# Optimization experiments

Measured on AMD Instinct MI355X. Metric: run time of the kernel, lower is better.

Reference implementation:

```python
import jax, jax.numpy as jnp
import numpy as np

EMB = 768
HEADS = 12
HEAD_DIM = EMB // HEADS
SCALE = HEAD_DIM ** -0.5


def setup_inputs() -> dict:
    key = jax.random.key(0)
    kq, kk, kv, kw = jax.random.split(key, 4)
    B, H, N, D = 2, HEADS, 2048, HEAD_DIM
    queries = jax.random.normal(kq, (B, H, N, D), dtype=jnp.float32)
    keys = jax.random.normal(kk, (B, H, N, D), dtype=jnp.float32)
    values = jax.random.normal(kv, (B, H, N, D), dtype=jnp.float32)
    proj_w = jax.random.normal(kw, (EMB, EMB), dtype=jnp.float32) * (EMB ** -0.5)
    proj_b = jnp.zeros((EMB,), dtype=jnp.float32)
    return {"queries": queries, "keys": keys, "values": values,
            "proj_w": proj_w, "proj_b": proj_b}


def reference(queries, keys, values, proj_w, proj_b):
    # energy: [b, h, n, n] -- full quadratic score matrix, as in the original
    energy = jnp.einsum('bhij,bhkj->bhik', queries, keys) * SCALE
    att = jax.nn.softmax(energy, axis=-1)  # att_drop_p=0.0 -> identity
    out = jnp.einsum('bhij,bhjk->bhik', att, values)  # [b, h, n, d]
    b, h, n, d = out.shape
    out = jnp.transpose(out, (0, 2, 1, 3)).reshape(b, n, h * d)  # 'b h n d -> b n (h d)'
    # nn.Linear: x @ W^T + b (projection dropout is inference identity)
    return out @ proj_w.T + proj_b
```

## Files before the change

kernel.cpp:

```cpp
#include <hip/hip_runtime.h>
#include <cstdint>

typedef short bf16x8 __attribute__((ext_vector_type(8)));
typedef float f32x4 __attribute__((ext_vector_type(4)));
typedef uint16_t u16x4 __attribute__((ext_vector_type(4)));

#define MFMA_16x16x32(a, b, c) __builtin_amdgcn_mfma_f32_16x16x32_bf16((a), (b), (c), 0, 0, 0)

static constexpr int BATCH = 2;
static constexpr int HEADS = 12;
static constexpr int NCTX  = 2048;
static constexpr int DH    = 64;
static constexpr int EMB   = 768;

static constexpr float QSCALE = 0.125f * 1.44269504088896340736f;

__device__ __forceinline__ uint16_t f2bf(float x) {
    uint32_t u = __float_as_uint(x);
    u += 0x7FFFu + ((u >> 16) & 1u);
    return (uint16_t)(u >> 16);
}
__device__ __forceinline__ uint32_t cvt_pk_bf16(float lo, float hi) {
    uint32_t r;
    asm("v_cvt_pk_bf16_f32 %0, %1, %2" : "=v"(r) : "v"(lo), "v"(hi));
    return r;
}

__global__ void k_cvt(const float* __restrict__ src, uint16_t* __restrict__ dst, int n4) {
    int i = blockIdx.x * blockDim.x + threadIdx.x;
    if (i >= n4) return;
    float4 v = reinterpret_cast<const float4*>(src)[i];
    u16x4 hv = {f2bf(v.x), f2bf(v.y), f2bf(v.z), f2bf(v.w)};
    reinterpret_cast<u16x4*>(dst)[i] = hv;
}

__global__ __launch_bounds__(256) void k_vt(const float* __restrict__ v,
                                            uint16_t* __restrict__ vt) {
    const int bh = blockIdx.y;
    const int n0 = blockIdx.x * 64;
    const int t  = threadIdx.x;
    __shared__ uint16_t tileT[64][72];

    const int r  = t >> 2;
    const int cc = (t & 3) * 16;
    const float* vp = v + ((size_t)bh * NCTX + n0 + r) * DH + cc;
#pragma unroll
    for (int u = 0; u < 4; ++u) {
        float4 x = reinterpret_cast<const float4*>(vp)[u];
        tileT[cc + 4 * u + 0][r] = f2bf(x.x);
        tileT[cc + 4 * u + 1][r] = f2bf(x.y);
        tileT[cc + 4 * u + 2][r] = f2bf(x.z);
        tileT[cc + 4 * u + 3][r] = f2bf(x.w);
    }
    __syncthreads();
    const int d  = t >> 2;
    const int nc = (t & 3) * 16;
    uint16_t* op = vt + ((size_t)bh * DH + d) * NCTX + n0 + nc;
#pragma unroll
    for (int u = 0; u < 2; ++u) {
        bf16x8 x = *reinterpret_cast<const bf16x8*>(&tileT[d][nc + 8 * u]);
        *reinterpret_cast<bf16x8*>(op + 8 * u) = x;
    }
}

__global__ __launch_bounds__(256) void k_attn(
        const float* __restrict__ q, const uint16_t* __restrict__ kb,
        const uint16_t* __restrict__ vt, uint16_t* __restrict__ xb) {
    const int bh = blockIdx.y;
    const int b  = bh / HEADS;
    const int h  = bh % HEADS;
    const int tid = threadIdx.x;
    const int w = tid >> 6;
    const int l = tid & 63;
    const int g = l >> 4;
    const int c = l & 15;

    __shared__ uint16_t K_s[2][64][72];
    __shared__ uint16_t V_s[2][64][72];
    __shared__ uint16_t P_s[4][16][72];

    const int q0 = blockIdx.x * 64 + w * 16;

    bf16x8 qa[2];
    {
        const float* qp = q + ((size_t)bh * NCTX + q0 + c) * DH + 8 * g;
#pragma unroll
        for (int kf = 0; kf < 2; ++kf) {
            float4 x0 = *reinterpret_cast<const float4*>(qp + kf * 32);
            float4 x1 = *reinterpret_cast<const float4*>(qp + kf * 32 + 4);
            bf16x8 f;
            f[0] = (short)f2bf(x0.x * QSCALE); f[1] = (short)f2bf(x0.y * QSCALE);
            f[2] = (short)f2bf(x0.z * QSCALE); f[3] = (short)f2bf(x0.w * QSCALE);
            f[4] = (short)f2bf(x1.x * QSCALE); f[5] = (short)f2bf(x1.y * QSCALE);
            f[6] = (short)f2bf(x1.z * QSCALE); f[7] = (short)f2bf(x1.w * QSCALE);
            qa[kf] = f;
        }
    }

    f32x4 zero = {0.f, 0.f, 0.f, 0.f};
    f32x4 o[4] = {zero, zero, zero, zero};
    float m = -1e30f;
    float lsum = 0.f;

    const int srow = tid >> 3;
    const int sch  = tid & 7;

    const uint16_t* kb_b = kb + (size_t)bh * NCTX * DH + srow * DH + sch * 8;
    const uint16_t* vt_b = vt + (size_t)bh * DH * NCTX + srow * NCTX + sch * 8;

    {
        bf16x8 a0 = *reinterpret_cast<const bf16x8*>(kb_b);
        bf16x8 a1 = *reinterpret_cast<const bf16x8*>(kb_b + 32 * DH);
        bf16x8 v0 = *reinterpret_cast<const bf16x8*>(vt_b);
        bf16x8 v1 = *reinterpret_cast<const bf16x8*>(vt_b + 32 * NCTX);
        *reinterpret_cast<bf16x8*>(&K_s[0][srow][sch * 8])      = a0;
        *reinterpret_cast<bf16x8*>(&K_s[0][srow + 32][sch * 8]) = a1;
        *reinterpret_cast<bf16x8*>(&V_s[0][srow][sch * 8])      = v0;
        *reinterpret_cast<bf16x8*>(&V_s[0][srow + 32][sch * 8]) = v1;
    }
    __syncthreads();

    for (int t = 0; t < NCTX / 64; ++t) {
        const int cur = t & 1;
        const int nxt = cur ^ 1;

        bf16x8 nk0, nk1, nv0, nv1;
        const bool pf = (t + 1) < NCTX / 64;
        if (pf) {
            const size_t ko = (size_t)(t + 1) * 64 * DH;
            const size_t vo = (size_t)(t + 1) * 64;
            nk0 = *reinterpret_cast<const bf16x8*>(kb_b + ko);
            nk1 = *reinterpret_cast<const bf16x8*>(kb_b + ko + 32 * DH);
            nv0 = *reinterpret_cast<const bf16x8*>(vt_b + vo);
            nv1 = *reinterpret_cast<const bf16x8*>(vt_b + vo + 32 * NCTX);
        }

        f32x4 s[4] = {zero, zero, zero, zero};
        __builtin_amdgcn_s_setprio(1);
#pragma unroll
        for (int nf = 0; nf < 4; ++nf) {
#pragma unroll
            for (int kf = 0; kf < 2; ++kf) {
                bf16x8 bhf = *reinterpret_cast<const bf16x8*>(&K_s[cur][nf * 16 + c][kf * 32 + 8 * g]);
                s[nf] = MFMA_16x16x32(bhf, qa[kf], s[nf]);
            }
        }
        __builtin_amdgcn_s_setprio(0);

        float smax = s[0][0];
#pragma unroll
        for (int nf = 0; nf < 4; ++nf)
#pragma unroll
            for (int r = 0; r < 4; ++r) smax = fmaxf(smax, s[nf][r]);
        smax = fmaxf(smax, __shfl_xor(smax, 16));
        smax = fmaxf(smax, __shfl_xor(smax, 32));

        if (!__all(smax <= m + 11.0f)) {
            float mnew = fmaxf(m, smax);
            float corr = __builtin_amdgcn_exp2f(m - mnew);
            m = mnew;
            lsum *= corr;
#pragma unroll
            for (int r = 0; r < 4; ++r) {
                float cr = __shfl(corr, 4 * g + r);
#pragma unroll
                for (int f = 0; f < 4; ++f) o[f][r] *= cr;
            }
        }

#pragma unroll
        for (int nf = 0; nf < 4; ++nf) {
            float p0 = __builtin_amdgcn_exp2f(s[nf][0] - m);
            float p1 = __builtin_amdgcn_exp2f(s[nf][1] - m);
            float p2 = __builtin_amdgcn_exp2f(s[nf][2] - m);
            float p3 = __builtin_amdgcn_exp2f(s[nf][3] - m);
            lsum += (p0 + p1) + (p2 + p3);
            uint2 pk;
            pk.x = cvt_pk_bf16(p0, p1);
            pk.y = cvt_pk_bf16(p2, p3);
            *reinterpret_cast<uint2*>(&P_s[w][c][16 * nf + 4 * g]) = pk;
        }

        bf16x8 pa0 = *reinterpret_cast<const bf16x8*>(&P_s[w][c][8 * g]);
        bf16x8 pa1 = *reinterpret_cast<const bf16x8*>(&P_s[w][c][32 + 8 * g]);
        __builtin_amdgcn_s_setprio(1);
#pragma unroll
        for (int f = 0; f < 4; ++f) {
            bf16x8 b0 = *reinterpret_cast<const bf16x8*>(&V_s[cur][f * 16 + c][8 * g]);
            bf16x8 b1 = *reinterpret_cast<const bf16x8*>(&V_s[cur][f * 16 + c][32 + 8 * g]);
            o[f] = MFMA_16x16x32(pa0, b0, o[f]);
            o[f] = MFMA_16x16x32(pa1, b1, o[f]);
        }
        __builtin_amdgcn_s_setprio(0);

        if (pf) {
            *reinterpret_cast<bf16x8*>(&K_s[nxt][srow][sch * 8])      = nk0;
            *reinterpret_cast<bf16x8*>(&K_s[nxt][srow + 32][sch * 8]) = nk1;
            *reinterpret_cast<bf16x8*>(&V_s[nxt][srow][sch * 8])      = nv0;
            *reinterpret_cast<bf16x8*>(&V_s[nxt][srow + 32][sch * 8]) = nv1;
        }
        __syncthreads();
    }

    lsum += __shfl_xor(lsum, 16);
    lsum += __shfl_xor(lsum, 32);
    const float linv = 1.0f / lsum;

    const size_t xbase = ((size_t)b * NCTX + q0) * EMB + h * DH;
#pragma unroll
    for (int r = 0; r < 4; ++r) {
        float lr = __shfl(linv, 4 * g + r);
#pragma unroll
        for (int f = 0; f < 4; ++f) {
            float v = o[f][r] * lr;
            size_t addr = xbase + (size_t)(4 * g + r) * EMB + f * 16 + c;
            xb[addr] = f2bf(v);
        }
    }
}

__global__ __launch_bounds__(256) void k_proj(
        const uint16_t* __restrict__ xb, const uint16_t* __restrict__ wb,
        const float* __restrict__ bias, float* __restrict__ out) {
    const int tid = threadIdx.x;
    const int w = tid >> 6;
    const int l = tid & 63;
    const int g = l >> 4;
    const int c = l & 15;
    const int m0 = blockIdx.x * 64 + w * 16;
    const int n0 = blockIdx.y * 64;

    __shared__ uint16_t Wh_s[64][40];

    f32x4 zero = {0.f, 0.f, 0.f, 0.f};
    f32x4 acc[4] = {zero, zero, zero, zero};

    const int srow = tid >> 2;
    const int sch  = tid & 3;
    constexpr int KSTEPS = EMB / 32;

    const uint16_t* whp = wb + (size_t)(n0 + srow) * EMB + sch * 8;
    const uint16_t* xhp = xb + (size_t)(m0 + c) * EMB + 8 * g;

    bf16x8 wldh = *reinterpret_cast<const bf16x8*>(whp);
    bf16x8 ah   = *reinterpret_cast<const bf16x8*>(xhp);

    for (int ks = 0; ks < KSTEPS; ++ks) {
        __syncthreads();
        *reinterpret_cast<bf16x8*>(&Wh_s[srow][sch * 8]) = wldh;
        __syncthreads();

        const int ksn = (ks + 1 < KSTEPS) ? (ks + 1) : (KSTEPS - 1);
        bf16x8 wldh_n = *reinterpret_cast<const bf16x8*>(whp + (size_t)ksn * 32);
        bf16x8 ah_n   = *reinterpret_cast<const bf16x8*>(xhp + (size_t)ksn * 32);

        __builtin_amdgcn_s_setprio(1);
#pragma unroll
        for (int nf = 0; nf < 4; ++nf) {
            bf16x8 bhf = *reinterpret_cast<const bf16x8*>(&Wh_s[nf * 16 + c][8 * g]);
            acc[nf] = MFMA_16x16x32(ah, bhf, acc[nf]);
        }
        __builtin_amdgcn_s_setprio(0);

        wldh = wldh_n; ah = ah_n;
    }

#pragma unroll
    for (int nf = 0; nf < 4; ++nf) {
#pragma unroll
        for (int r = 0; r < 4; ++r) {
            int row = m0 + g * 4 + r;
            int col = n0 + nf * 16 + c;
            out[(size_t)row * EMB + col] = acc[nf][r] + bias[col];
        }
    }
}

extern "C" void kernel_launch(void* const* d_in, const int* in_sizes, int n_in,
                              void* d_out, int out_size, void* d_ws, size_t ws_size,
                              hipStream_t stream) {
    const float* q    = (const float*)d_in[0];
    const float* k    = (const float*)d_in[1];
    const float* v    = (const float*)d_in[2];
    const float* pw   = (const float*)d_in[3];
    const float* pb   = (const float*)d_in[4];
    float* out = (float*)d_out;

    const size_t nqkv = (size_t)BATCH * HEADS * NCTX * DH;
    const size_t nx   = (size_t)BATCH * NCTX * EMB;
    const size_t nw   = (size_t)EMB * EMB;

    uint8_t* ws = (uint8_t*)d_ws;
    uint16_t* kb = (uint16_t*)ws;              ws += nqkv * 2;
    uint16_t* vt = (uint16_t*)ws;              ws += nqkv * 2;
    uint16_t* xb = (uint16_t*)ws;              ws += nx * 2;
    uint16_t* wb = (uint16_t*)ws;              ws += nw * 2;

    k_cvt<<<(int)(nqkv / 4 / 256), 256, 0, stream>>>(k, kb, (int)(nqkv / 4));
    k_cvt<<<(int)(nw / 4 / 256),   256, 0, stream>>>(pw, wb, (int)(nw / 4));
    k_vt<<<dim3(NCTX / 64, BATCH * HEADS), 256, 0, stream>>>(v, vt);

    k_attn<<<dim3(NCTX / 64, BATCH * HEADS), 256, 0, stream>>>(q, kb, vt, xb);

    k_proj<<<dim3((BATCH * NCTX) / 64, EMB / 64), 256, 0, stream>>>(xb, wb, pb, out);
}
```

Before: 83.66 us.

## Merge conversion launches, defer softmax max shuffles, double k-step in projection

The two bf16 conversion kernels for K and the projection weight are merged into one launch, which removes one kernel launch and its tail. In the attention loop, the per-lane row max is computed first and the cross-lane shuffles run only when the lazy-rescale check fails, taking shuffles off the common path. The projection GEMM now stages 64-wide K chunks per barrier pair instead of 32, halving the barriers and global load rounds at the cost of more LDS and registers. The lazy-rescale check now uses the per-lane max, which is equivalent because __all spans the whole wave.

```diff
diff --git a/kernel.cpp b/kernel.cpp
--- a/kernel.cpp
+++ b/kernel.cpp
@@ -26,12 +26,19 @@
     return r;
 }
 
-__global__ void k_cvt(const float* __restrict__ src, uint16_t* __restrict__ dst, int n4) {
+__global__ void k_cvt2(const float* __restrict__ a, uint16_t* __restrict__ da, int n4a,
+                       const float* __restrict__ b2, uint16_t* __restrict__ db, int n4b) {
     int i = blockIdx.x * blockDim.x + threadIdx.x;
-    if (i >= n4) return;
-    float4 v = reinterpret_cast<const float4*>(src)[i];
+    const float* src; uint16_t* dst; int j;
+    if (i < n4a) { src = a; dst = da; j = i; }
+    else {
+        j = i - n4a;
+        if (j >= n4b) return;
+        src = b2; dst = db;
+    }
+    float4 v = reinterpret_cast<const float4*>(src)[j];
     u16x4 hv = {f2bf(v.x), f2bf(v.y), f2bf(v.z), f2bf(v.w)};
-    reinterpret_cast<u16x4*>(dst)[i] = hv;
+    reinterpret_cast<u16x4*>(dst)[j] = hv;
 }
 
 __global__ __launch_bounds__(256) void k_vt(const float* __restrict__ v,
@@ -147,15 +154,15 @@
         }
         __builtin_amdgcn_s_setprio(0);
 
-        float smax = s[0][0];
-#pragma unroll
-        for (int nf = 0; nf < 4; ++nf)
-#pragma unroll
-            for (int r = 0; r < 4; ++r) smax = fmaxf(smax, s[nf][r]);
-        smax = fmaxf(smax, __shfl_xor(smax, 16));
-        smax = fmaxf(smax, __shfl_xor(smax, 32));
-
-        if (!__all(smax <= m + 11.0f)) {
+        float pm0 = fmaxf(fmaxf(s[0][0], s[0][1]), fmaxf(s[0][2], s[0][3]));
+        float pm1 = fmaxf(fmaxf(s[1][0], s[1][1]), fmaxf(s[1][2], s[1][3]));
+        float pm2 = fmaxf(fmaxf(s[2][0], s[2][1]), fmaxf(s[2][2], s[2][3]));
+        float pm3 = fmaxf(fmaxf(s[3][0], s[3][1]), fmaxf(s[3][2], s[3][3]));
+        float pmax = fmaxf(fmaxf(pm0, pm1), fmaxf(pm2, pm3));
+
+        if (!__all(pmax <= m + 11.0f)) {
+            float smax = fmaxf(pmax, __shfl_xor(pmax, 16));
+            smax = fmaxf(smax, __shfl_xor(smax, 32));
             float mnew = fmaxf(m, smax);
             float corr = __builtin_amdgcn_exp2f(m - mnew);
             m = mnew;
@@ -230,39 +237,46 @@
     const int m0 = blockIdx.x * 64 + w * 16;
     const int n0 = blockIdx.y * 64;
 
-    __shared__ uint16_t Wh_s[64][40];
+    __shared__ uint16_t W_s[64][72];
 
     f32x4 zero = {0.f, 0.f, 0.f, 0.f};
     f32x4 acc[4] = {zero, zero, zero, zero};
 
     const int srow = tid >> 2;
     const int sch  = tid & 3;
-    constexpr int KSTEPS = EMB / 32;
+    constexpr int ROUNDS = EMB / 64;
 
     const uint16_t* whp = wb + (size_t)(n0 + srow) * EMB + sch * 8;
     const uint16_t* xhp = xb + (size_t)(m0 + c) * EMB + 8 * g;
 
-    bf16x8 wldh = *reinterpret_cast<const bf16x8*>(whp);
-    bf16x8 ah   = *reinterpret_cast<const bf16x8*>(xhp);
-
-    for (int ks = 0; ks < KSTEPS; ++ks) {
+    bf16x8 w0 = *reinterpret_cast<const bf16x8*>(whp);
+    bf16x8 w1 = *reinterpret_cast<const bf16x8*>(whp + 32);
+    bf16x8 a0 = *reinterpret_cast<const bf16x8*>(xhp);
+    bf16x8 a1 = *reinterpret_cast<const bf16x8*>(xhp + 32);
+
+    for (int rd = 0; rd < ROUNDS; ++rd) {
         __syncthreads();
-        *reinterpret_cast<bf16x8*>(&Wh_s[srow][sch * 8]) = wldh;
+        *reinterpret_cast<bf16x8*>(&W_s[srow][sch * 8])      = w0;
+        *reinterpret_cast<bf16x8*>(&W_s[srow][32 + sch * 8]) = w1;
         __syncthreads();
 
-        const int ksn = (ks + 1 < KSTEPS) ? (ks + 1) : (KSTEPS - 1);
-        bf16x8 wldh_n = *reinterpret_cast<const bf16x8*>(whp + (size_t)ksn * 32);
-        bf16x8 ah_n   = *reinterpret_cast<const bf16x8*>(xhp + (size_t)ksn * 32);
+        const int rn = (rd + 1 < ROUNDS) ? (rd + 1) : (ROUNDS - 1);
+        bf16x8 w0n = *reinterpret_cast<const bf16x8*>(whp + (size_t)rn * 64);
+        bf16x8 w1n = *reinterpret_cast<const bf16x8*>(whp + (size_t)rn * 64 + 32);
+        bf16x8 a0n = *reinterpret_cast<const bf16x8*>(xhp + (size_t)rn * 64);
+        bf16x8 a1n = *reinterpret_cast<const bf16x8*>(xhp + (size_t)rn * 64 + 32);
 
         __builtin_amdgcn_s_setprio(1);
 #pragma unroll
         for (int nf = 0; nf < 4; ++nf) {
-            bf16x8 bhf = *reinterpret_cast<const bf16x8*>(&Wh_s[nf * 16 + c][8 * g]);
-            acc[nf] = MFMA_16x16x32(ah, bhf, acc[nf]);
+            bf16x8 b0 = *reinterpret_cast<const bf16x8*>(&W_s[nf * 16 + c][8 * g]);
+            bf16x8 b1 = *reinterpret_cast<const bf16x8*>(&W_s[nf * 16 + c][32 + 8 * g]);
+            acc[nf] = MFMA_16x16x32(a0, b0, acc[nf]);
+            acc[nf] = MFMA_16x16x32(a1, b1, acc[nf]);
         }
         __builtin_amdgcn_s_setprio(0);
 
-        wldh = wldh_n; ah = ah_n;
+        w0 = w0n; w1 = w1n; a0 = a0n; a1 = a1n;
     }
 
 #pragma unroll
@@ -296,8 +310,9 @@
     uint16_t* xb = (uint16_t*)ws;              ws += nx * 2;
     uint16_t* wb = (uint16_t*)ws;              ws += nw * 2;
 
-    k_cvt<<<(int)(nqkv / 4 / 256), 256, 0, stream>>>(k, kb, (int)(nqkv / 4));
-    k_cvt<<<(int)(nw / 4 / 256),   256, 0, stream>>>(pw, wb, (int)(nw / 4));
+    const int n4k = (int)(nqkv / 4);
+    const int n4w = (int)(nw / 4);
+    k_cvt2<<<(n4k + n4w + 255) / 256, 256, 0, stream>>>(k, kb, n4k, pw, wb, n4w);
     k_vt<<<dim3(NCTX / 64, BATCH * HEADS), 256, 0, stream>>>(v, vt);
 
     k_attn<<<dim3(NCTX / 64, BATCH * HEADS), 256, 0, stream>>>(q, kb, vt, xb);
```

Result: faster. 78.28 us (-6.4%).
